# Kernel tuning notes

Measured on AMD Instinct MI355X. Metric: run time of the kernel, lower is better.

## Reference

```python
import jax, jax.numpy as jnp
import numpy as np

D_MODEL = 1024
N_HEADS = 16
MLP_DIM = 4096


def _layernorm(x, g, b, eps=1e-5):
    mu = jnp.mean(x, axis=-1, keepdims=True)
    var = jnp.var(x, axis=-1, keepdims=True)
    return (x - mu) * jax.lax.rsqrt(var + eps) * g + b


def setup_inputs() -> dict:
    key = jax.random.key(0)
    ks = jax.random.split(key, 12)
    B, S, D, F = 2, 2048, D_MODEL, MLP_DIM
    s = 1.0 / np.sqrt(D)
    sf = 1.0 / np.sqrt(F)
    return {
        "x": jax.random.normal(ks[0], (B, S, D), jnp.float32),
        "ln1_g": jnp.ones((D,), jnp.float32),
        "ln1_b": jnp.zeros((D,), jnp.float32),
        "w_q": jax.random.uniform(ks[1], (D, D), jnp.float32, -s, s),
        "w_k": jax.random.uniform(ks[2], (D, D), jnp.float32, -s, s),
        "w_v": jax.random.uniform(ks[3], (D, D), jnp.float32, -s, s),
        "w_o": jax.random.uniform(ks[4], (D, D), jnp.float32, -s, s),
        "b_o": jax.random.uniform(ks[5], (D,), jnp.float32, -s, s),
        "ln2_g": jnp.ones((D,), jnp.float32),
        "ln2_b": jnp.zeros((D,), jnp.float32),
        "w1": jax.random.uniform(ks[6], (D, F), jnp.float32, -s, s),
        "b1": jax.random.uniform(ks[7], (F,), jnp.float32, -s, s),
        "w2": jax.random.uniform(ks[8], (F, D), jnp.float32, -sf, sf),
        "b2": jax.random.uniform(ks[9], (D,), jnp.float32, -sf, sf),
    }


def reference(x, ln1_g, ln1_b, w_q, w_k, w_v, w_o, b_o, ln2_g, ln2_b, w1, b1, w2, b2):
    B, S, D = x.shape
    H = N_HEADS
    hd = D // H
    # --- attention sublayer (pre-LN, residual) ---
    h = _layernorm(x, ln1_g, ln1_b)
    q = (h @ w_q).reshape(B, S, H, hd).transpose(0, 2, 1, 3)  # [B,H,S,hd]
    k = (h @ w_k).reshape(B, S, H, hd).transpose(0, 2, 1, 3)
    v = (h @ w_v).reshape(B, S, H, hd).transpose(0, 2, 1, 3)
    scores = jnp.einsum('bhqd,bhkd->bhqk', q, k) / np.sqrt(hd)  # [B,H,S,S]
    attn = jax.nn.softmax(scores, axis=-1)
    out = jnp.einsum('bhqk,bhkd->bhqd', attn, v)
    out = out.transpose(0, 2, 1, 3).reshape(B, S, D)
    x = out @ w_o + b_o + x
    # --- MLP sublayer (pre-LN, residual) ---
    h = _layernorm(x, ln2_g, ln2_b)
    h = jax.nn.gelu(h @ w1 + b1, approximate=False)
    return h @ w2 + b2 + x
```

## Files before the change

kernel.cpp:

```cpp
#include <hip/hip_runtime.h>
#include <math.h>


typedef __attribute__((ext_vector_type(8))) short s8v;
typedef __attribute__((ext_vector_type(4))) short s4v;
typedef __attribute__((ext_vector_type(4))) float f4v;
typedef __attribute__((ext_vector_type(16))) float f16v;

#define M_ROWS 4096
#define DM 1024
#define FF 4096
#define QKV_LD 3072

__device__ inline short f2bf(float f) {
  unsigned u = __builtin_bit_cast(unsigned, f);
  u += 0x7fff + ((u >> 16) & 1);
  return (short)(u >> 16);
}
__device__ inline float bf2f(short s) {
  unsigned u = ((unsigned)(unsigned short)s) << 16;
  return __builtin_bit_cast(float, u);
}

__device__ inline void gload_lds16(const void* g, void* lds) {
  __builtin_amdgcn_global_load_lds(
      (const __attribute__((address_space(1))) unsigned*)(uintptr_t)g,
      (__attribute__((address_space(3))) unsigned*)(unsigned)(uintptr_t)lds,
      16, 0, 0);
}

__device__ inline s4v ds_tr16(unsigned off) {
  s4v r;
  asm volatile("ds_read_b64_tr_b16 %0, %1" : "=v"(r) : "v"(off));
  return r;
}

__device__ inline s8v cat8(s4v a, s4v b) {
  return __builtin_shufflevector(a, b, 0, 1, 2, 3, 4, 5, 6, 7);
}

__device__ inline unsigned pkbf(float a, float b) {
  unsigned r;
  asm("v_cvt_pk_bf16_f32 %0, %1, %2" : "=v"(r) : "v"(a), "v"(b));
  return r;
}

__device__ inline float gelu_t(float x) {
  float x3 = x * x * x;
  float z = fmaf(x3, 0.044715f, x) * 1.5957691216f;
  float e = __expf(z);
  float th = fmaf(-2.0f, __frcp_rn(e + 1.0f), 1.0f);
  return 0.5f * x * (1.0f + th);
}

__global__ void wt_kernel(const float* __restrict__ W, short* __restrict__ Wt,
                          int K, int N) {
  __shared__ float tile[32][33];
  int tx = threadIdx.x, ty = threadIdx.y;
  int n0 = blockIdx.x * 32, k0 = blockIdx.y * 32;
#pragma unroll
  for (int i = 0; i < 4; ++i)
    tile[ty + 8 * i][tx] = W[(size_t)(k0 + ty + 8 * i) * N + n0 + tx];
  __syncthreads();
#pragma unroll
  for (int i = 0; i < 4; ++i)
    Wt[(size_t)(n0 + ty + 8 * i) * K + k0 + tx] = f2bf(tile[tx][ty + 8 * i]);
}

__global__ __launch_bounds__(256) void ln_kernel(const float* __restrict__ x,
                                                 const float* __restrict__ g,
                                                 const float* __restrict__ b,
                                                 short* __restrict__ out) {
  int row = blockIdx.x, tid = threadIdx.x;
  const float4* xr = (const float4*)(x + (size_t)row * DM);
  float4 v = xr[tid];
  float s = v.x + v.y + v.z + v.w;
  float q = v.x * v.x + v.y * v.y + v.z * v.z + v.w * v.w;
#pragma unroll
  for (int off = 32; off; off >>= 1) {
    s += __shfl_down(s, off);
    q += __shfl_down(q, off);
  }
  __shared__ float red[8];
  if ((tid & 63) == 0) { red[tid >> 6] = s; red[4 + (tid >> 6)] = q; }
  __syncthreads();
  if (tid == 0) {
    float S = red[0] + red[1] + red[2] + red[3];
    float Q = red[4] + red[5] + red[6] + red[7];
    float mean = S * (1.0f / DM);
    float var = Q * (1.0f / DM) - mean * mean;
    red[0] = mean;
    red[1] = rsqrtf(var + 1e-5f);
  }
  __syncthreads();
  float mean = red[0], rstd = red[1];
  float4 gv = ((const float4*)g)[tid], bv = ((const float4*)b)[tid];
  s4v o;
  o[0] = f2bf((v.x - mean) * rstd * gv.x + bv.x);
  o[1] = f2bf((v.y - mean) * rstd * gv.y + bv.y);
  o[2] = f2bf((v.z - mean) * rstd * gv.z + bv.z);
  o[3] = f2bf((v.w - mean) * rstd * gv.w + bv.w);
  *(s4v*)&out[(size_t)row * DM + tid * 4] = o;
}

template <int EPI>
__global__ __launch_bounds__(256) void gemm_kernel(
    const short* __restrict__ A, const short* __restrict__ Bt,
    const float* __restrict__ bias, const float* __restrict__ res,
    void* __restrict__ Cout, int M, int N, int K) {
  __shared__ short As[2][128 * 64];
  __shared__ short Bs[2][128 * 64];
  int tid = threadIdx.x, lane = tid & 63, wave = tid >> 6;
  int wr = wave >> 1, wc = wave & 1;
  int l16 = lane & 15, lhi = lane >> 4;
  int row0 = blockIdx.y * 128, col0 = blockIdx.x * 128;
  int lrow = lane >> 3, lcol8 = (lane & 7) * 8;

  const f4v fzero = {0.f, 0.f, 0.f, 0.f};
  f4v acc[4][4];
#pragma unroll
  for (int m = 0; m < 4; ++m)
#pragma unroll
    for (int n = 0; n < 4; ++n) acc[m][n] = fzero;

  const int nt = K >> 6;

#pragma unroll
  for (int i = 0; i < 4; ++i) {
    int ch = wave * 4 + i;
    int row = ch * 8 + lrow;
    gload_lds16(&A[(size_t)(row0 + row) * K + lcol8], &As[0][ch * 512]);
    gload_lds16(&Bt[(size_t)(col0 + row) * K + lcol8], &Bs[0][ch * 512]);
  }
  __syncthreads();

  for (int t = 0; t < nt; ++t) {
    int cur = t & 1, nxt = cur ^ 1;
    if (t + 1 < nt) {
      int k1 = (t + 1) << 6;
#pragma unroll
      for (int i = 0; i < 4; ++i) {
        int ch = wave * 4 + i;
        int row = ch * 8 + lrow;
        gload_lds16(&A[(size_t)(row0 + row) * K + k1 + lcol8], &As[nxt][ch * 512]);
        gload_lds16(&Bt[(size_t)(col0 + row) * K + k1 + lcol8], &Bs[nxt][ch * 512]);
      }
    }
#pragma unroll
    for (int kk = 0; kk < 2; ++kk) {
      s8v af[4], bfr[4];
#pragma unroll
      for (int m = 0; m < 4; ++m)
        af[m] = *(const s8v*)&As[cur][(wr * 64 + m * 16 + l16) * 64 + kk * 32 + lhi * 8];
#pragma unroll
      for (int n = 0; n < 4; ++n)
        bfr[n] = *(const s8v*)&Bs[cur][(wc * 64 + n * 16 + l16) * 64 + kk * 32 + lhi * 8];
#pragma unroll
      for (int m = 0; m < 4; ++m)
#pragma unroll
        for (int n = 0; n < 4; ++n)
          acc[m][n] = __builtin_amdgcn_mfma_f32_16x16x32_bf16(af[m], bfr[n],
                                                              acc[m][n], 0, 0, 0);
    }
    __syncthreads();
  }

#pragma unroll
  for (int m = 0; m < 4; ++m)
#pragma unroll
    for (int n = 0; n < 4; ++n)
#pragma unroll
      for (int r = 0; r < 4; ++r) {
        int row = row0 + wr * 64 + m * 16 + lhi * 4 + r;
        int col = col0 + wc * 64 + n * 16 + l16;
        size_t idx = (size_t)row * N + col;
        float v = acc[m][n][r];
        if (EPI == 0) {
          ((short*)Cout)[idx] = f2bf(v);
        } else if (EPI == 1) {
          ((float*)Cout)[idx] = v + bias[col] + res[idx];
        } else {
          ((short*)Cout)[idx] = f2bf(gelu_t(v + bias[col]));
        }
      }
}

__global__ __launch_bounds__(512) void attn_kernel(const short* __restrict__ q,
                                                   const short* __restrict__ k,
                                                   const short* __restrict__ v,
                                                   short* __restrict__ opart,
                                                   float2* __restrict__ ml) {
  __shared__ short Ks[2][64 * 64];
  __shared__ short Vt[2][64 * 64];
  int tid = threadIdx.x, lane = tid & 63, w = tid >> 6;
  int l31 = lane & 31, l15 = lane & 15, h = lane >> 5;
  int qb = blockIdx.x * 256;
  int bh = blockIdx.y;
  int sp = blockIdx.z;
  int b = bh >> 4, hh = bh & 15;
  const size_t rbase = (size_t)b * 2048 * QKV_LD + (size_t)hh * 64;
  const float S2 = 0.18033688f;
  const int kbase = sp * 1024;

  int krow = w * 8 + (lane >> 3);
  int kcol = (((lane & 7) ^ (krow & 7)) * 8);
  int vnb = w >> 1, vrem = (w & 1) * 64 + lane;
  int vkey = vrem >> 1, vc8 = vrem & 1;

#define STAGE_KV(buf, kt)                                                      \
  {                                                                            \
    gload_lds16(&k[rbase + (size_t)((kt) + krow) * QKV_LD + kcol],             \
                &Ks[buf][w * 512]);                                            \
    gload_lds16(&v[rbase + (size_t)((kt) + vkey) * QKV_LD + vnb * 16 + vc8 * 8], \
                &Vt[buf][w * 512]);                                            \
  }

  int qrow = qb + w * 32 + l31;
  s8v qf[4];
#pragma unroll
  for (int c = 0; c < 4; ++c)
    qf[c] = *(const s8v*)&q[rbase + (size_t)qrow * QKV_LD + c * 16 + h * 8];

  f16v o0, o1;
#pragma unroll
  for (int i = 0; i < 16; ++i) { o0[i] = 0.f; o1[i] = 0.f; }
  float mreg = -3.0e38f, lsum = 0.f;

  STAGE_KV(0, kbase);
  __syncthreads();

  for (int t = 0; t < 16; ++t) {
    int cur = t & 1;
    if (t + 1 < 16) STAGE_KV(cur ^ 1, kbase + (t + 1) * 64);
    unsigned vtb = (unsigned)(uintptr_t)&Vt[cur][0];

    f16v t0, t1;
#pragma unroll
    for (int i = 0; i < 16; ++i) { t0[i] = 0.f; t1[i] = 0.f; }
    __builtin_amdgcn_s_setprio(1);
#pragma unroll
    for (int c = 0; c < 4; ++c) {
      int slot = ((2 * c + h) ^ (l31 & 7)) * 8;
      s8v k0f = *(const s8v*)&Ks[cur][l31 * 64 + slot];
      s8v k1f = *(const s8v*)&Ks[cur][(32 + l31) * 64 + slot];
      t0 = __builtin_amdgcn_mfma_f32_32x32x16_bf16(k0f, qf[c], t0, 0, 0, 0);
      t1 = __builtin_amdgcn_mfma_f32_32x32x16_bf16(k1f, qf[c], t1, 0, 0, 0);
    }
    __builtin_amdgcn_s_setprio(0);

    float mx[8];
#pragma unroll
    for (int i = 0; i < 8; ++i)
      mx[i] = fmaxf(fmaxf(t0[i], t0[i + 8]), fmaxf(t1[i], t1[i + 8]));
    float rm = fmaxf(fmaxf(fmaxf(mx[0], mx[1]), fmaxf(mx[2], mx[3])),
                     fmaxf(fmaxf(mx[4], mx[5]), fmaxf(mx[6], mx[7])));
    rm = fmaxf(rm, __shfl_xor(rm, 32));
    if (!__all(rm <= mreg + 64.0f)) {
      float newm = fmaxf(mreg, rm);
      float sc = exp2f((mreg - newm) * S2);
      mreg = newm;
#pragma unroll
      for (int i = 0; i < 16; ++i) { o0[i] *= sc; o1[i] *= sc; }
      lsum *= sc;
    }
    float ms2 = mreg * S2;
#pragma unroll
    for (int i = 0; i < 16; ++i) {
      t0[i] = exp2f(fmaf(t0[i], S2, -ms2));
      t1[i] = exp2f(fmaf(t1[i], S2, -ms2));
    }
    float sm[8];
#pragma unroll
    for (int i = 0; i < 8; ++i)
      sm[i] = (t0[i] + t0[i + 8]) + (t1[i] + t1[i + 8]);
    float rs = ((sm[0] + sm[1]) + (sm[2] + sm[3])) +
               ((sm[4] + sm[5]) + (sm[6] + sm[7]));
    rs += __shfl_xor(rs, 32);
    lsum += rs;

    s8v pB[4];
#pragma unroll
    for (int c = 0; c < 4; ++c) {
      int rb = (c & 1) * 8;
      float e0, e1, e2, e3, e4, e5, e6, e7;
      if (c < 2) {
        e0 = t0[rb]; e1 = t0[rb + 1]; e2 = t0[rb + 2]; e3 = t0[rb + 3];
        e4 = t0[rb + 4]; e5 = t0[rb + 5]; e6 = t0[rb + 6]; e7 = t0[rb + 7];
      } else {
        e0 = t1[rb]; e1 = t1[rb + 1]; e2 = t1[rb + 2]; e3 = t1[rb + 3];
        e4 = t1[rb + 4]; e5 = t1[rb + 5]; e6 = t1[rb + 6]; e7 = t1[rb + 7];
      }
      unsigned wA0 = pkbf(e0, e1), wA1 = pkbf(e2, e3);
      unsigned wB0 = pkbf(e4, e5), wB1 = pkbf(e6, e7);
      unsigned s0 = h ? wA0 : wB0, s1 = h ? wA1 : wB1;
      unsigned r0 = __shfl_xor(s0, 32), r1 = __shfl_xor(s1, 32);
      uint4 ww;
      ww.x = h ? r0 : wA0;
      ww.y = h ? r1 : wA1;
      ww.z = h ? wB0 : r0;
      ww.w = h ? wB1 : r1;
      pB[c] = __builtin_bit_cast(s8v, ww);
    }

    s4v va[2][4][2];
#pragma unroll
    for (int db = 0; db < 2; ++db) {
      unsigned base = vtb + (unsigned)(db * 2 + (l31 >> 4)) * 2048 + 2u * l15;
#pragma unroll
      for (int c = 0; c < 4; ++c) {
        unsigned a = base + (unsigned)(c * 512 + h * 256);
        va[db][c][0] = ds_tr16(a);
        va[db][c][1] = ds_tr16(a + 128);
      }
    }
    asm volatile("s_waitcnt lgkmcnt(0)");
    __builtin_amdgcn_sched_barrier(0);
    __builtin_amdgcn_s_setprio(1);
#pragma unroll
    for (int c = 0; c < 4; ++c) {
      o0 = __builtin_amdgcn_mfma_f32_32x32x16_bf16(cat8(va[0][c][0], va[0][c][1]),
                                                   pB[c], o0, 0, 0, 0);
      o1 = __builtin_amdgcn_mfma_f32_32x32x16_bf16(cat8(va[1][c][0], va[1][c][1]),
                                                   pB[c], o1, 0, 0, 0);
    }
    __builtin_amdgcn_s_setprio(0);
    __syncthreads();
  }

  size_t rowg = (size_t)b * 2048 + qrow;
  size_t obase = (size_t)sp * 4096 * 1024 + rowg * 1024 + hh * 64;
#pragma unroll
  for (int db = 0; db < 2; ++db)
#pragma unroll
    for (int qq = 0; qq < 4; ++qq) {
      s4v pv;
#pragma unroll
      for (int i = 0; i < 4; ++i)
        pv[i] = f2bf(db == 0 ? o0[qq * 4 + i] : o1[qq * 4 + i]);
      *(s4v*)&opart[obase + db * 32 + qq * 8 + h * 4] = pv;
    }
  if (h == 0) ml[(size_t)sp * 65536 + rowg * 16 + hh] = make_float2(mreg, lsum);
#undef STAGE_KV
}

__global__ __launch_bounds__(256) void attn_combine(const short* __restrict__ op,
                                                    const float2* __restrict__ ml,
                                                    short* __restrict__ o) {
  int row = blockIdx.x, t = threadIdx.x;
  int head = t >> 4;
  const float S2 = 0.18033688f;
  float2 ml0 = ml[(size_t)row * 16 + head];
  float2 ml1 = ml[65536 + (size_t)row * 16 + head];
  float M = fmaxf(ml0.x, ml1.x);
  float a0 = exp2f((ml0.x - M) * S2);
  float a1 = exp2f((ml1.x - M) * S2);
  float inv = 1.0f / fmaf(ml0.y, a0, ml1.y * a1);
  a0 *= inv; a1 *= inv;
  s4v v0 = *(const s4v*)&op[(size_t)row * 1024 + t * 4];
  s4v v1 = *(const s4v*)&op[(size_t)4096 * 1024 + row * 1024 + t * 4];
  s4v pv;
#pragma unroll
  for (int i = 0; i < 4; ++i)
    pv[i] = f2bf(bf2f(v0[i]) * a0 + bf2f(v1[i]) * a1);
  *(s4v*)&o[(size_t)row * 1024 + t * 4] = pv;
}

extern "C" void kernel_launch(void* const* d_in, const int* in_sizes, int n_in,
                              void* d_out, int out_size, void* d_ws, size_t ws_size,
                              hipStream_t stream) {
  (void)in_sizes; (void)n_in; (void)out_size; (void)ws_size;
  const float* x    = (const float*)d_in[0];
  const float* ln1g = (const float*)d_in[1];
  const float* ln1b = (const float*)d_in[2];
  const float* wq   = (const float*)d_in[3];
  const float* wk   = (const float*)d_in[4];
  const float* wv   = (const float*)d_in[5];
  const float* wo   = (const float*)d_in[6];
  const float* bo   = (const float*)d_in[7];
  const float* ln2g = (const float*)d_in[8];
  const float* ln2b = (const float*)d_in[9];
  const float* w1   = (const float*)d_in[10];
  const float* b1   = (const float*)d_in[11];
  const float* w2   = (const float*)d_in[12];
  const float* b2   = (const float*)d_in[13];
  float* out = (float*)d_out;

  char* ws = (char*)d_ws;
  const size_t MB = 1024 * 1024;
  short* h1   = (short*)(ws);
  short* qkv  = (short*)(ws + 8 * MB);
  short* mid  = (short*)(ws);
  short* at   = (short*)(ws + 32 * MB);
  short* h2   = (short*)(ws + 32 * MB);
  float* x2   = (float*)(ws + 40 * MB);
  short* opart = (short*)(ws + 40 * MB);
  float2* mlb  = (float2*)(ws);
  short* wqkvT = (short*)(ws + 56 * MB);
  short* wqT  = wqkvT;
  short* wkT  = wqkvT + 1024 * 1024;
  short* wvT  = wqkvT + 2 * 1024 * 1024;
  short* woT  = (short*)(ws + 62 * MB);
  short* w1T  = (short*)(ws + 64 * MB);
  short* w2T  = (short*)(ws + 72 * MB);

  dim3 tb(32, 8);
  wt_kernel<<<dim3(32, 32), tb, 0, stream>>>(wq, wqT, 1024, 1024);
  wt_kernel<<<dim3(32, 32), tb, 0, stream>>>(wk, wkT, 1024, 1024);
  wt_kernel<<<dim3(32, 32), tb, 0, stream>>>(wv, wvT, 1024, 1024);
  wt_kernel<<<dim3(32, 32), tb, 0, stream>>>(wo, woT, 1024, 1024);
  wt_kernel<<<dim3(128, 32), tb, 0, stream>>>(w1, w1T, 1024, 4096);
  wt_kernel<<<dim3(32, 128), tb, 0, stream>>>(w2, w2T, 4096, 1024);

  ln_kernel<<<M_ROWS, 256, 0, stream>>>(x, ln1g, ln1b, h1);

  gemm_kernel<0><<<dim3(24, 32), 256, 0, stream>>>(h1, wqkvT, nullptr, nullptr,
                                                   qkv, M_ROWS, QKV_LD, DM);

  attn_kernel<<<dim3(8, 32, 2), 512, 0, stream>>>(qkv, qkv + 1024, qkv + 2048,
                                                  opart, mlb);
  attn_combine<<<4096, 256, 0, stream>>>(opart, mlb, at);

  gemm_kernel<1><<<dim3(8, 32), 256, 0, stream>>>(at, woT, bo, x, x2, M_ROWS, DM, DM);

  ln_kernel<<<M_ROWS, 256, 0, stream>>>(x2, ln2g, ln2b, h2);

  gemm_kernel<2><<<dim3(32, 32), 256, 0, stream>>>(h2, w1T, b1, nullptr, mid,
                                                   M_ROWS, FF, DM);

  gemm_kernel<1><<<dim3(8, 32), 256, 0, stream>>>(mid, w2T, b2, x2, out,
                                                  M_ROWS, DM, FF);
}
```

Measured before the change: 276.9 us.

## Stage GEMM epilogue through LDS for vectorized stores; batch weight transposes; cheaper GELU

The GEMM epilogue now writes accumulators into shared memory in two halves, then each thread reads contiguous rows and issues vectorized float4/8xbf16 global stores, with vectorized bias and residual loads. Before, each thread did scattered scalar stores. The four 1024x1024 weight transposes are merged into one launch using blockIdx.z. GELU is rewritten in sigmoid form as x/(1+exp2(...)), which removes some arithmetic. The staging adds extra barriers and reuses the As buffer, which must be large enough for a 64x128 float tile.

```diff
diff --git a/kernel.cpp b/kernel.cpp
--- a/kernel.cpp
+++ b/kernel.cpp
@@ -45,12 +45,11 @@
   return r;
 }
 
-__device__ inline float gelu_t(float x) {
-  float x3 = x * x * x;
-  float z = fmaf(x3, 0.044715f, x) * 1.5957691216f;
-  float e = __expf(z);
-  float th = fmaf(-2.0f, __frcp_rn(e + 1.0f), 1.0f);
-  return 0.5f * x * (1.0f + th);
+__device__ inline float gelu_s(float x) {
+  float t = x * x;
+  float z = fmaf(t, -0.10296333f, -2.88539008f);
+  float e = exp2f(x * z);
+  return x * __frcp_rn(1.0f + e);
 }
 
 __global__ void wt_kernel(const float* __restrict__ W, short* __restrict__ Wt,
@@ -65,6 +64,25 @@
 #pragma unroll
   for (int i = 0; i < 4; ++i)
     Wt[(size_t)(n0 + ty + 8 * i) * K + k0 + tx] = f2bf(tile[tx][ty + 8 * i]);
+}
+
+__global__ void wt4_kernel(const float* __restrict__ w0, const float* __restrict__ w1,
+                           const float* __restrict__ w2, const float* __restrict__ w3,
+                           short* __restrict__ o0, short* __restrict__ o1,
+                           short* __restrict__ o2, short* __restrict__ o3) {
+  __shared__ float tile[32][33];
+  int tx = threadIdx.x, ty = threadIdx.y;
+  int n0 = blockIdx.x * 32, k0 = blockIdx.y * 32;
+  int zz = blockIdx.z;
+  const float* W = zz == 0 ? w0 : zz == 1 ? w1 : zz == 2 ? w2 : w3;
+  short* Wt = zz == 0 ? o0 : zz == 1 ? o1 : zz == 2 ? o2 : o3;
+#pragma unroll
+  for (int i = 0; i < 4; ++i)
+    tile[ty + 8 * i][tx] = W[(size_t)(k0 + ty + 8 * i) * 1024 + n0 + tx];
+  __syncthreads();
+#pragma unroll
+  for (int i = 0; i < 4; ++i)
+    Wt[(size_t)(n0 + ty + 8 * i) * 1024 + k0 + tx] = f2bf(tile[tx][ty + 8 * i]);
 }
 
 __global__ __launch_bounds__(256) void ln_kernel(const float* __restrict__ x,
@@ -165,24 +183,55 @@
     __syncthreads();
   }
 
-#pragma unroll
-  for (int m = 0; m < 4; ++m)
-#pragma unroll
-    for (int n = 0; n < 4; ++n)
-#pragma unroll
-      for (int r = 0; r < 4; ++r) {
-        int row = row0 + wr * 64 + m * 16 + lhi * 4 + r;
-        int col = col0 + wc * 64 + n * 16 + l16;
-        size_t idx = (size_t)row * N + col;
-        float v = acc[m][n][r];
-        if (EPI == 0) {
-          ((short*)Cout)[idx] = f2bf(v);
-        } else if (EPI == 1) {
-          ((float*)Cout)[idx] = v + bias[col] + res[idx];
+  float* Cl = (float*)&As[0][0];
+  const float4* Cl4 = (const float4*)Cl;
+  int r2 = tid >> 2, cs = (tid & 3) * 32;
+#pragma unroll
+  for (int hf = 0; hf < 2; ++hf) {
+    if (wr == hf) {
+#pragma unroll
+      for (int m = 0; m < 4; ++m)
+#pragma unroll
+        for (int n = 0; n < 4; ++n)
+#pragma unroll
+          for (int r = 0; r < 4; ++r)
+            Cl[(m * 16 + lhi * 4 + r) * 128 + wc * 64 + n * 16 + l16] = acc[m][n][r];
+    }
+    __syncthreads();
+    int grow = row0 + hf * 64 + r2;
+    if (EPI == 1) {
+#pragma unroll
+      for (int j = 0; j < 8; ++j) {
+        float4 v = Cl4[r2 * 32 + (cs >> 2) + j];
+        float4 bb = ((const float4*)bias)[(col0 + cs) / 4 + j];
+        float4 rr = ((const float4*)res)[((size_t)grow * N + col0 + cs) / 4 + j];
+        float4 o;
+        o.x = v.x + bb.x + rr.x; o.y = v.y + bb.y + rr.y;
+        o.z = v.z + bb.z + rr.z; o.w = v.w + bb.w + rr.w;
+        ((float4*)Cout)[((size_t)grow * N + col0 + cs) / 4 + j] = o;
+      }
+    } else {
+#pragma unroll
+      for (int j2 = 0; j2 < 4; ++j2) {
+        float4 a = Cl4[r2 * 32 + (cs >> 2) + 2 * j2];
+        float4 b = Cl4[r2 * 32 + (cs >> 2) + 2 * j2 + 1];
+        float e[8] = {a.x, a.y, a.z, a.w, b.x, b.y, b.z, b.w};
+        s8v o;
+        if (EPI == 2) {
+          float4 b0 = ((const float4*)bias)[(col0 + cs) / 4 + 2 * j2];
+          float4 b1 = ((const float4*)bias)[(col0 + cs) / 4 + 2 * j2 + 1];
+          float bb[8] = {b0.x, b0.y, b0.z, b0.w, b1.x, b1.y, b1.z, b1.w};
+#pragma unroll
+          for (int i = 0; i < 8; ++i) o[i] = f2bf(gelu_s(e[i] + bb[i]));
         } else {
-          ((short*)Cout)[idx] = f2bf(gelu_t(v + bias[col]));
+#pragma unroll
+          for (int i = 0; i < 8; ++i) o[i] = f2bf(e[i]);
         }
+        *(s8v*)&((short*)Cout)[(size_t)grow * N + col0 + cs + j2 * 8] = o;
       }
+    }
+    __syncthreads();
+  }
 }
 
 __global__ __launch_bounds__(512) void attn_kernel(const short* __restrict__ q,
@@ -404,10 +453,8 @@
   short* w2T  = (short*)(ws + 72 * MB);
 
   dim3 tb(32, 8);
-  wt_kernel<<<dim3(32, 32), tb, 0, stream>>>(wq, wqT, 1024, 1024);
-  wt_kernel<<<dim3(32, 32), tb, 0, stream>>>(wk, wkT, 1024, 1024);
-  wt_kernel<<<dim3(32, 32), tb, 0, stream>>>(wv, wvT, 1024, 1024);
-  wt_kernel<<<dim3(32, 32), tb, 0, stream>>>(wo, woT, 1024, 1024);
+  wt4_kernel<<<dim3(32, 32, 4), tb, 0, stream>>>(wq, wk, wv, wo,
+                                                 wqT, wkT, wvT, woT);
   wt_kernel<<<dim3(128, 32), tb, 0, stream>>>(w1, w1T, 1024, 4096);
   wt_kernel<<<dim3(32, 128), tb, 0, stream>>>(w2, w2T, 4096, 1024);
 
```

Measured after the change: 294.9 us. +6.5%, slower.
